# Kernel tuning notes

Measured on AMD Instinct MI355X. Metric: run time of the kernel, lower is better.

## Reference

```python
import math
import jax, jax.numpy as jnp
import numpy as np

NUM_BUCKETS = 32
MAX_DISTANCE = 128
N_HEADS = 16
D_KV = 64


def relative_position_bucket(rel_pos, num_buckets=NUM_BUCKETS, max_distance=MAX_DISTANCE):
    # bidirectional=True path of the original
    n = -rel_pos
    nb = num_buckets // 2
    ret = (n < 0).astype(jnp.int32) * nb
    n = jnp.abs(n)
    max_exact = nb // 2
    is_small = n < max_exact
    val_large = max_exact + (
        jnp.log(n.astype(jnp.float32) / max_exact)
        / math.log(max_distance / max_exact)
        * (nb - max_exact)
    ).astype(jnp.int32)
    val_large = jnp.minimum(val_large, nb - 1)
    return jnp.where(is_small, n, val_large) + ret


def setup_inputs() -> dict:
    key = jax.random.key(0)
    ks = jax.random.split(key, 6)
    B, S, D = 2, 2048, 1024
    inner = N_HEADS * D_KV  # 1024
    sc = 1.0 / math.sqrt(D)
    return {
        "x": jax.random.normal(ks[0], (B, S, D), dtype=jnp.float32),
        "Wq": jax.random.normal(ks[1], (D, inner), dtype=jnp.float32) * sc,
        "Wk": jax.random.normal(ks[2], (D, inner), dtype=jnp.float32) * sc,
        "Wv": jax.random.normal(ks[3], (D, inner), dtype=jnp.float32) * sc,
        "Wo": jax.random.normal(ks[4], (inner, D), dtype=jnp.float32) * sc,
        "rel_table": jax.random.normal(ks[5], (NUM_BUCKETS, N_HEADS), dtype=jnp.float32),
        "attention_mask": jnp.zeros((B, 1, 1, S), dtype=jnp.float32),
    }


def reference(x, Wq, Wk, Wv, Wo, rel_table, attention_mask):
    B, S, D = x.shape
    H, Dk = N_HEADS, D_KV

    q = (x @ Wq).reshape(B, S, H, Dk).transpose(0, 2, 1, 3)  # bhqd
    k = (x @ Wk).reshape(B, S, H, Dk).transpose(0, 2, 1, 3)
    v = (x @ Wv).reshape(B, S, H, Dk).transpose(0, 2, 1, 3)

    # NOTE: T5 attention has no 1/sqrt(d) scaling
    scores = jnp.einsum('bhqd,bhkd->bhqk', q.astype(jnp.float32), k.astype(jnp.float32))

    pos = jnp.arange(S)
    rel_pos = pos[None, :] - pos[:, None]  # [S,S] = k_pos - q_pos
    buckets = relative_position_bucket(rel_pos)
    position_bias = jnp.transpose(rel_table[buckets], (2, 0, 1))  # [H,S,S]

    scores = scores + position_bias[None, ...] + attention_mask
    weights = jax.nn.softmax(scores, axis=-1)
    out = jnp.einsum('bhqk,bhkd->bhqd', weights, v.astype(jnp.float32))
    out = out.transpose(0, 2, 1, 3).reshape(B, S, H * Dk).astype(x.dtype)
    out = out @ Wo
    return (out, position_bias)
```

## Files before the change

kernel.cpp:

```cpp
#include <hip/hip_runtime.h>
#include <hip/hip_bf16.h>
#include <math.h>
#include <stdint.h>

typedef __bf16 bf16_t;
typedef __attribute__((ext_vector_type(8))) __bf16 bf16x8;
typedef __attribute__((ext_vector_type(4))) float f32x4;
typedef float f32x4a __attribute__((ext_vector_type(4), aligned(4)));
typedef unsigned short u16;
typedef unsigned int u32;

#define DEV static __device__ __forceinline__
#define LOG2E 1.4426950408889634f

DEV u16 f2b(float f){ bf16_t h = (bf16_t)f; return __builtin_bit_cast(u16, h); }
DEV float b2f(u16 u){ bf16_t h = __builtin_bit_cast(bf16_t, u); return (float)h; }
DEV f32x4 mfma16(bf16x8 a, bf16x8 b, f32x4 c){
  return __builtin_amdgcn_mfma_f32_16x16x32_bf16(a, b, c, 0, 0, 0);
}

#if __has_builtin(__builtin_amdgcn_exp2f)
DEV float fexp2(float x){ return __builtin_amdgcn_exp2f(x); }
#else
DEV float fexp2(float x){ return exp2f(x); }
#endif

DEV void gld16(const void* g, void* l){
  __builtin_amdgcn_global_load_lds((const __attribute__((address_space(1))) u32*)g,
                                   (__attribute__((address_space(3))) u32*)l, 16, 0, 0);
}

DEV bf16x8 ldsA64(const u16* arr, int row, int ch){
  return *(const bf16x8*)&arr[row*64 + ((ch ^ (row&7))*8)];
}
DEV bf16x8 ldsA32(const u16* arr, int row, int ch){
  return *(const bf16x8*)&arr[row*32 + ((ch ^ ((row>>1)&3))*8)];
}

__global__ __launch_bounds__(256) void k_prep(const float* __restrict__ x,
                                              const float* __restrict__ Wq, const float* __restrict__ Wk,
                                              const float* __restrict__ Wv, const float* __restrict__ Wo,
                                              const float* __restrict__ rel_table, const float* __restrict__ mask,
                                              u16* __restrict__ xh, u16* __restrict__ xl,
                                              u16* __restrict__ wth, u16* __restrict__ wot,
                                              float* __restrict__ bt, float* __restrict__ bt2,
                                              float* __restrict__ msk2){
  __shared__ float tile[64][65];
  int bid = blockIdx.x;
  int t = threadIdx.x;
  if(bid < 4096){
    size_t i = ((size_t)bid*256 + t)*4;
    float4 v = *(const float4*)(x + i);
    ushort4 hv, lv; float f, hf;
    f=v.x; hv.x=f2b(f); hf=b2f(hv.x); lv.x=f2b(f-hf);
    f=v.y; hv.y=f2b(f); hf=b2f(hv.y); lv.y=f2b(f-hf);
    f=v.z; hv.z=f2b(f); hf=b2f(hv.z); lv.z=f2b(f-hf);
    f=v.w; hv.w=f2b(f); hf=b2f(hv.w); lv.w=f2b(f-hf);
    *(ushort4*)(xh+i) = hv;
    *(ushort4*)(xl+i) = lv;
  } else if(bid < 5120){
    int rr = bid - 4096;
    int z = rr >> 8, ky = (rr >> 4) & 15, nx = rr & 15;
    const float* W = (z==0)?Wq:((z==1)?Wk:((z==2)?Wv:Wo));
    int n0 = nx*64, k0 = ky*64;
    int r = t>>6, c = t&63;
    #pragma unroll
    for(int i=0;i<16;i++){
      int row = i*4 + r;
      tile[row][c] = W[(size_t)(k0+row)*1024 + n0 + c];
    }
    __syncthreads();
    #pragma unroll
    for(int i=0;i<16;i++){
      int nrow = i*4 + r;
      float v = tile[c][nrow];
      size_t o = (size_t)(n0+nrow)*1024 + k0 + c;
      if(z<3) wth[(size_t)z*1048576 + o] = f2b(v);
      else    wot[o] = f2b(v);
    }
  } else {
    int gid = (bid-5120)*256 + t;
    if(gid < 4096) msk2[gid] = mask[gid]*LOG2E;
    int h = gid >> 12, idx = gid & 4095;
    float v = 0.f;
    if(idx < 4095){
      int delta = idx - 2047;
      int n = -delta;
      int ret = 0;
      if(n < 0){ ret = 16; n = -n; }
      int bucket;
      if(n < 8) bucket = n + ret;
      else {
        float a = (float)log((double)n * 0.125);
        float rr2 = (float)((double)a / (double)2.7725887298583984f);
        int vl = 8 + (int)(rr2 * 8.0f);
        vl = vl > 15 ? 15 : vl;
        bucket = vl + ret;
      }
      v = rel_table[bucket*16 + h];
    }
    bt[gid] = v;
    bt2[gid] = v*LOG2E - 32.0f;
  }
}

__global__ __launch_bounds__(256) void k_gemm_qkv(const u16* __restrict__ xh, const u16* __restrict__ xl,
                                                  const u16* __restrict__ wth,
                                                  u16* __restrict__ qh, u16* __restrict__ ql,
                                                  u16* __restrict__ kh, u16* __restrict__ vt){
  __shared__ __align__(16) u16 SM[24576];
  int z = blockIdx.z;
  const u16* WH = wth + (size_t)z*1048576;
  int lin2 = blockIdx.x + 8*blockIdx.y;
  int nl2 = (lin2 & 7)*32 + (lin2 >> 3);
  int n0 = (nl2 & 7)*128, m0 = (nl2 >> 3)*128;
  int t = threadIdx.x, w = t>>6, lane = t&63, l16 = lane&15, g = lane>>4;
  f32x4 acc[4][4];
  #pragma unroll
  for(int i=0;i<4;i++)
    #pragma unroll
    for(int j=0;j<4;j++) acc[i][j] = {0.f,0.f,0.f,0.f};
  int rbase = (w>>1)*64, cbase = (w&1)*64;

  #pragma unroll
  for(int jj=0;jj<6;jj++){
    int q = w + 4*jj;
    int arr = q>>3, sub = q&7;
    if(z!=0 && arr==1) continue;
    int row = sub*16 + (lane>>2);
    int lch = (lane&3) ^ ((row>>1)&3);
    const u16* src;
    if(arr==0)      src = xh + (size_t)(m0+row)*1024 + lch*8;
    else if(arr==1) src = xl + (size_t)(m0+row)*1024 + lch*8;
    else            src = WH + (size_t)(n0+row)*1024 + lch*8;
    gld16(src, &SM[q*512]);
  }
  __syncthreads();

  for(int it=0; it<32; ++it){
    const u16* Ah = SM + (it&1)*12288;
    const u16* Al = Ah + 4096;
    const u16* Bh = Ah + 8192;
    if(it < 31){
      u16* dstb = SM + ((it+1)&1)*12288;
      int kn = (it+1)*32;
      #pragma unroll
      for(int jj=0;jj<6;jj++){
        int q = w + 4*jj;
        int arr = q>>3, sub = q&7;
        if(z!=0 && arr==1) continue;
        int row = sub*16 + (lane>>2);
        int lch = (lane&3) ^ ((row>>1)&3);
        const u16* src;
        if(arr==0)      src = xh + (size_t)(m0+row)*1024 + kn + lch*8;
        else if(arr==1) src = xl + (size_t)(m0+row)*1024 + kn + lch*8;
        else            src = WH + (size_t)(n0+row)*1024 + kn + lch*8;
        gld16(src, dstb + q*512);
      }
      __builtin_amdgcn_sched_barrier(0);
    }
    if(z!=0){
      bf16x8 ah[4];
      #pragma unroll
      for(int i=0;i<4;i++) ah[i] = ldsA32(Ah, rbase + i*16 + l16, g);
      #pragma unroll
      for(int j=0;j<4;j++){
        bf16x8 bh = ldsA32(Bh, cbase + j*16 + l16, g);
        #pragma unroll
        for(int i=0;i<4;i++)
          acc[i][j] = mfma16(ah[i], bh, acc[i][j]);
      }
    } else {
      bf16x8 ah[4], am[4];
      #pragma unroll
      for(int i=0;i<4;i++){
        int row = rbase + i*16 + l16;
        ah[i] = ldsA32(Ah, row, g);
        am[i] = ldsA32(Al, row, g);
      }
      #pragma unroll
      for(int j=0;j<4;j++){
        bf16x8 bh = ldsA32(Bh, cbase + j*16 + l16, g);
        #pragma unroll
        for(int i=0;i<4;i++){
          acc[i][j] = mfma16(ah[i], bh, acc[i][j]);
          acc[i][j] = mfma16(am[i], bh, acc[i][j]);
        }
      }
    }
    __syncthreads();
  }
  if(z==2){
    #pragma unroll
    for(int i=0;i<4;i++)
      #pragma unroll
      for(int j=0;j<4;j++)
        #pragma unroll
        for(int r=0;r<4;r++){
          int ml = rbase + i*16 + g*4 + r;
          int nl = cbase + j*16 + l16;
          SM[nl*136 + ml] = f2b(acc[i][j][r]);
        }
    __syncthreads();
    int bb = m0 >> 11;
    #pragma unroll
    for(int kk=0;kk<8;kk++){
      int id = t + 256*kk;
      int row = id>>4, ch = id&15;
      uint4 v = *(const uint4*)&SM[row*136 + ch*8];
      int n = n0 + row;
      size_t dst = ((size_t)(bb*16 + (n>>6))*64 + (n&63))*2048 + (m0&2047) + ch*8;
      *(uint4*)&vt[dst] = v;
    }
  } else {
    #pragma unroll
    for(int i=0;i<4;i++)
      #pragma unroll
      for(int j=0;j<4;j++)
        #pragma unroll
        for(int r=0;r<4;r++){
          int m = m0 + rbase + i*16 + g*4 + r;
          int n = n0 + cbase + j*16 + l16;
          float v = acc[i][j][r];
          if(z==0) v *= LOG2E;
          int b = m >> 11, s = m & 2047;
          int hh = n >> 6, d = n & 63;
          size_t a = ((size_t)(b*16+hh)*2048 + s)*64 + d;
          u16 hb = f2b(v);
          if(z==0){ qh[a]=hb; ql[a]=f2b(v - b2f(hb)); }
          else    { kh[a]=hb; }
        }
  }
}

__global__ __launch_bounds__(256,4) void k_attn(const u16* __restrict__ qh, const u16* __restrict__ ql,
                                              const u16* __restrict__ kh,
                                              const u16* __restrict__ vt, const float* __restrict__ bt2,
                                              const float* __restrict__ msk2,
                                              const float* __restrict__ bt, float* __restrict__ bias_out,
                                              u16* __restrict__ ao){
  __shared__ __align__(16) u16 SM[20480];
  int lin = blockIdx.x + 32*blockIdx.y;
  int nlw = (lin & 7)*128 + (lin >> 3);
  int qx = nlw & 31, bh = nlw >> 5;
  int b = bh>>4, h = bh&15;
  int q0 = qx*64;
  int t = threadIdx.x, w = t>>6, lane = t&63, l16 = lane&15, g = lane>>4;
  size_t base  = (size_t)bh*2048*64;
  size_t vbase = (size_t)bh*64*2048;
  u16* PSw = SM + 16384 + w*1024;
  const float* bt2h = bt2 + h*4096;
  const float* msk2b = msk2 + b*2048;
  size_t wbase = ((size_t)(bh*32 + qx))*65536 + t*8;

  bf16x8 qfh[2], qfl[2];
  {
    int qr = q0 + w*16 + l16;
    size_t a0 = base + (size_t)qr*64 + g*8;
    qfh[0] = *(const bf16x8*)&qh[a0];
    qfl[0] = *(const bf16x8*)&ql[a0];
    qfh[1] = *(const bf16x8*)&qh[a0+32];
    qfl[1] = *(const bf16x8*)&ql[a0+32];
  }
  f32x4 O[4];
  float rs[4];
  #pragma unroll
  for(int jd=0;jd<4;jd++) O[jd] = {0.f,0.f,0.f,0.f};
  #pragma unroll
  for(int r=0;r<4;r++) rs[r] = 0.f;
  int qgbase = q0 + w*16 + g*4;

  f32x4a bv0, bv1;
  {
    size_t f = wbase;
    int hh = (int)(f >> 22);
    int rem = (int)(f & 4194303);
    int qq = rem >> 11;
    int kk = rem & 2047;
    const float* row = bt + hh*4096 + (kk - qq + 2047);
    bv0 = *(const f32x4a*)(row);
    bv1 = *(const f32x4a*)(row + 4);
  }
  #pragma unroll
  for(int jj=0;jj<4;jj++){
    int q = w + 4*jj;
    int arr = q>>3, sub = q&7;
    int row = sub*8 + (lane>>3);
    int lch = (lane&7) ^ (row&7);
    const u16* src = (arr==0) ? kh + base + (size_t)row*64 + lch*8
                              : vt + vbase + (size_t)row*2048 + lch*8;
    gld16(src, &SM[q*512]);
  }
  __syncthreads();

  for(int it=0; it<32; ++it){
    int k0 = it*64;
    const u16* KH = SM + (it&1)*8192;
    const u16* VT = KH + 4096;
    if(it < 31){
      u16* dstb = SM + ((it+1)&1)*8192;
      int kn = k0 + 64;
      #pragma unroll
      for(int jj=0;jj<4;jj++){
        int q = w + 4*jj;
        int arr = q>>3, sub = q&7;
        int row = sub*8 + (lane>>3);
        int lch = (lane&7) ^ (row&7);
        const u16* src = (arr==0) ? kh + base + (size_t)(kn+row)*64 + lch*8
                                  : vt + vbase + (size_t)row*2048 + kn + lch*8;
        gld16(src, dstb + q*512);
      }
      __builtin_amdgcn_sched_barrier(0);
    }
    f32x4 sc[4];
    {
      const float* bb = bt2h + (k0 + l16 + 2047 - qgbase);
      #pragma unroll
      for(int j=0;j<4;j++){
        f32x4a ld = *(const f32x4a*)(bb + j*16 - 3);
        float mk = msk2b[k0 + j*16 + l16];
        sc[j] = (f32x4){ld[3]+mk, ld[2]+mk, ld[1]+mk, ld[0]+mk};
      }
    }
    {
      size_t f = wbase + (size_t)it*2048;
      __builtin_nontemporal_store(bv0, (f32x4a*)(bias_out + f));
      __builtin_nontemporal_store(bv1, (f32x4a*)(bias_out + f + 4));
      if(it < 31){
        size_t fn = f + 2048;
        int hh = (int)(fn >> 22);
        int rem = (int)(fn & 4194303);
        int qq = rem >> 11;
        int kk = rem & 2047;
        const float* row = bt + hh*4096 + (kk - qq + 2047);
        bv0 = *(const f32x4a*)(row);
        bv1 = *(const f32x4a*)(row + 4);
      }
    }
    __builtin_amdgcn_s_setprio(1);
    #pragma unroll
    for(int j=0;j<4;j++){
      int krow = j*16 + l16;
      bf16x8 kfh0 = ldsA64(KH, krow, g);
      bf16x8 kfh1 = ldsA64(KH, krow, 4+g);
      f32x4 s = sc[j];
      s = mfma16(qfh[0], kfh0, s);
      s = mfma16(qfl[0], kfh0, s);
      s = mfma16(qfh[1], kfh1, s);
      s = mfma16(qfl[1], kfh1, s);
      sc[j] = s;
    }
    __builtin_amdgcn_s_setprio(0);
    #pragma unroll
    for(int j=0;j<4;j++){
      #pragma unroll
      for(int r=0;r<4;r++){
        float p = fexp2(sc[j][r]);
        rs[r] += p;
        int rowp = g*4 + r;
        int colp = j*16 + l16;
        PSw[rowp*64 + (((colp>>3) ^ (rowp&7))*8) + (colp&7)] = f2b(p);
      }
    }
    __builtin_amdgcn_s_setprio(1);
    #pragma unroll
    for(int ds=0; ds<2; ds++){
      bf16x8 pa = ldsA64(PSw, l16, ds*4 + g);
      #pragma unroll
      for(int jd=0;jd<4;jd++){
        bf16x8 vb = ldsA64(VT, jd*16 + l16, ds*4 + g);
        O[jd] = mfma16(pa, vb, O[jd]);
      }
    }
    __builtin_amdgcn_s_setprio(0);
    __syncthreads();
  }
  #pragma unroll
  for(int r=0;r<4;r++){
    float v = rs[r];
    v += __shfl_xor(v,1,64);
    v += __shfl_xor(v,2,64);
    v += __shfl_xor(v,4,64);
    v += __shfl_xor(v,8,64);
    float inv = 1.f/v;
    int q = qgbase + r;
    size_t a = ((size_t)(b*2048 + q))*1024 + h*64;
    #pragma unroll
    for(int jd=0;jd<4;jd++)
      ao[a + jd*16 + l16] = f2b(O[jd][r]*inv);
  }
}

__global__ __launch_bounds__(256) void k_gemm_out(const u16* __restrict__ ao, const u16* __restrict__ wot,
                                                  float* __restrict__ out){
  __shared__ __align__(16) u16 SM[16384];
  int lin2 = blockIdx.x + 8*blockIdx.y;
  int nl2 = (lin2 & 7)*32 + (lin2 >> 3);
  int n0 = (nl2 & 7)*128, m0 = (nl2 >> 3)*128;
  int t = threadIdx.x, w = t>>6, lane = t&63, l16 = lane&15, g = lane>>4;
  f32x4 acc[4][4];
  #pragma unroll
  for(int i=0;i<4;i++)
    #pragma unroll
    for(int j=0;j<4;j++) acc[i][j] = {0.f,0.f,0.f,0.f};
  int rbase = (w>>1)*64, cbase = (w&1)*64;

  #pragma unroll
  for(int jj=0;jj<4;jj++){
    int q = w + 4*jj;
    int arr = q>>3, sub = q&7;
    int row = sub*16 + (lane>>2);
    int lch = (lane&3) ^ ((row>>1)&3);
    const u16* src = (arr==0) ? ao  + (size_t)(m0+row)*1024 + lch*8
                              : wot + (size_t)(n0+row)*1024 + lch*8;
    gld16(src, &SM[q*512]);
  }
  __syncthreads();

  for(int it=0; it<32; ++it){
    const u16* As = SM + (it&1)*8192;
    const u16* Bs = As + 4096;
    if(it < 31){
      u16* dstb = SM + ((it+1)&1)*8192;
      int kn = (it+1)*32;
      #pragma unroll
      for(int jj=0;jj<4;jj++){
        int q = w + 4*jj;
        int arr = q>>3, sub = q&7;
        int row = sub*16 + (lane>>2);
        int lch = (lane&3) ^ ((row>>1)&3);
        const u16* src = (arr==0) ? ao  + (size_t)(m0+row)*1024 + kn + lch*8
                                  : wot + (size_t)(n0+row)*1024 + kn + lch*8;
        gld16(src, dstb + q*512);
      }
      __builtin_amdgcn_sched_barrier(0);
    }
    bf16x8 af[4];
    #pragma unroll
    for(int i=0;i<4;i++) af[i] = ldsA32(As, rbase + i*16 + l16, g);
    #pragma unroll
    for(int j=0;j<4;j++){
      bf16x8 bfb = ldsA32(Bs, cbase + j*16 + l16, g);
      #pragma unroll
      for(int i=0;i<4;i++)
        acc[i][j] = mfma16(af[i], bfb, acc[i][j]);
    }
    __syncthreads();
  }
  #pragma unroll
  for(int i=0;i<4;i++)
    #pragma unroll
    for(int j=0;j<4;j++)
      #pragma unroll
      for(int r=0;r<4;r++){
        int m = m0 + rbase + i*16 + g*4 + r;
        int n = n0 + cbase + j*16 + l16;
        __builtin_nontemporal_store(acc[i][j][r], &out[(size_t)m*1024 + n]);
      }
}

extern "C" void kernel_launch(void* const* d_in, const int* in_sizes, int n_in,
                              void* d_out, int out_size, void* d_ws, size_t ws_size,
                              hipStream_t stream) {
  const float* x   = (const float*)d_in[0];
  const float* Wq  = (const float*)d_in[1];
  const float* Wk  = (const float*)d_in[2];
  const float* Wv  = (const float*)d_in[3];
  const float* Wo  = (const float*)d_in[4];
  const float* rel = (const float*)d_in[5];
  const float* msk = (const float*)d_in[6];
  float* out = (float*)d_out;
  float* bias_out = out + (size_t)4194304;
  char* ws = (char*)d_ws;
  u16* xh  = (u16*)(ws + 0);
  u16* xl  = (u16*)(ws + 8388608);
  u16* wth = (u16*)(ws + 16777216);
  u16* wot = (u16*)(ws + 23068672);
  u16* qh  = (u16*)(ws + 25165824);
  u16* ql  = (u16*)(ws + 33554432);
  u16* kh  = (u16*)(ws + 41943040);
  u16* vt  = (u16*)(ws + 50331648);
  u16* ao  = (u16*)(ws + 58720256);
  float* bt  = (float*)(ws + 67108864);
  float* bt2 = (float*)(ws + 67371008);
  float* msk2= (float*)(ws + 67633152);

  k_prep      <<<5376, 256, 0, stream>>>(x, Wq, Wk, Wv, Wo, rel, msk,
                                         xh, xl, wth, wot, bt, bt2, msk2);
  k_gemm_qkv  <<<dim3(8,32,3), 256, 0, stream>>>(xh, xl, wth, qh, ql, kh, vt);
  k_attn      <<<dim3(32,32), 256, 0, stream>>>(qh, ql, kh, vt, bt2, msk2, bt, bias_out, ao);
  k_gemm_out  <<<dim3(8,32), 256, 0, stream>>>(ao, wot, out);
}
```

Baseline: 442.3 us.

## Transpose QK MFMA operands in attention and shrink output GEMM N-tile

After: 435.9 us, median of 2. No clear change (-1.5%).

```diff
diff --git a/kernel.cpp b/kernel.cpp
--- a/kernel.cpp
+++ b/kernel.cpp
@@ -263,11 +263,11 @@
     qfl[1] = *(const bf16x8*)&ql[a0+32];
   }
   f32x4 O[4];
-  float rs[4];
+  float rs4[4];
   #pragma unroll
   for(int jd=0;jd<4;jd++) O[jd] = {0.f,0.f,0.f,0.f};
   #pragma unroll
-  for(int r=0;r<4;r++) rs[r] = 0.f;
+  for(int r=0;r<4;r++) rs4[r] = 0.f;
   int qgbase = q0 + w*16 + g*4;
 
   f32x4a bv0, bv1;
@@ -314,12 +314,13 @@
     }
     f32x4 sc[4];
     {
-      const float* bb = bt2h + (k0 + l16 + 2047 - qgbase);
+      const float* bb = bt2h + (k0 + g*4 + 2047 - (q0 + w*16 + l16));
+      const float* mm = msk2b + k0 + g*4;
       #pragma unroll
       for(int j=0;j<4;j++){
-        f32x4a ld = *(const f32x4a*)(bb + j*16 - 3);
-        float mk = msk2b[k0 + j*16 + l16];
-        sc[j] = (f32x4){ld[3]+mk, ld[2]+mk, ld[1]+mk, ld[0]+mk};
+        f32x4a bvv = *(const f32x4a*)(bb + j*16);
+        f32x4a mvv = *(const f32x4a*)(mm + j*16);
+        sc[j] = (f32x4){bvv[0]+mvv[0], bvv[1]+mvv[1], bvv[2]+mvv[2], bvv[3]+mvv[3]};
       }
     }
     {
@@ -344,23 +345,22 @@
       bf16x8 kfh0 = ldsA64(KH, krow, g);
       bf16x8 kfh1 = ldsA64(KH, krow, 4+g);
       f32x4 s = sc[j];
-      s = mfma16(qfh[0], kfh0, s);
-      s = mfma16(qfl[0], kfh0, s);
-      s = mfma16(qfh[1], kfh1, s);
-      s = mfma16(qfl[1], kfh1, s);
+      s = mfma16(kfh0, qfh[0], s);
+      s = mfma16(kfh0, qfl[0], s);
+      s = mfma16(kfh1, qfh[1], s);
+      s = mfma16(kfh1, qfl[1], s);
       sc[j] = s;
     }
     __builtin_amdgcn_s_setprio(0);
     #pragma unroll
     for(int j=0;j<4;j++){
-      #pragma unroll
-      for(int r=0;r<4;r++){
-        float p = fexp2(sc[j][r]);
-        rs[r] += p;
-        int rowp = g*4 + r;
-        int colp = j*16 + l16;
-        PSw[rowp*64 + (((colp>>3) ^ (rowp&7))*8) + (colp&7)] = f2b(p);
-      }
+      float p0 = fexp2(sc[j][0]); rs4[0] += p0;
+      float p1 = fexp2(sc[j][1]); rs4[1] += p1;
+      float p2 = fexp2(sc[j][2]); rs4[2] += p2;
+      float p3 = fexp2(sc[j][3]); rs4[3] += p3;
+      ushort4 us = { f2b(p0), f2b(p1), f2b(p2), f2b(p3) };
+      int ch = (j*2 + (g>>1)) ^ (l16 & 7);
+      *(ushort4*)&PSw[l16*64 + ch*8 + (g&1)*4] = us;
     }
     __builtin_amdgcn_s_setprio(1);
     #pragma unroll
@@ -375,14 +375,12 @@
     __builtin_amdgcn_s_setprio(0);
     __syncthreads();
   }
+  float tot = (rs4[0]+rs4[1]) + (rs4[2]+rs4[3]);
+  tot += __shfl_xor(tot, 16, 64);
+  tot += __shfl_xor(tot, 32, 64);
   #pragma unroll
   for(int r=0;r<4;r++){
-    float v = rs[r];
-    v += __shfl_xor(v,1,64);
-    v += __shfl_xor(v,2,64);
-    v += __shfl_xor(v,4,64);
-    v += __shfl_xor(v,8,64);
-    float inv = 1.f/v;
+    float inv = 1.f/__shfl(tot, g*4+r, 64);
     int q = qgbase + r;
     size_t a = ((size_t)(b*2048 + q))*1024 + h*64;
     #pragma unroll
@@ -393,20 +391,20 @@
 
 __global__ __launch_bounds__(256) void k_gemm_out(const u16* __restrict__ ao, const u16* __restrict__ wot,
                                                   float* __restrict__ out){
-  __shared__ __align__(16) u16 SM[16384];
-  int lin2 = blockIdx.x + 8*blockIdx.y;
-  int nl2 = (lin2 & 7)*32 + (lin2 >> 3);
-  int n0 = (nl2 & 7)*128, m0 = (nl2 >> 3)*128;
+  __shared__ __align__(16) u16 SM[12288];
+  int lin2 = blockIdx.x + 16*blockIdx.y;
+  int nl2 = (lin2 & 7)*64 + (lin2 >> 3);
+  int n0 = (nl2 & 15)*64, m0 = (nl2 >> 4)*128;
   int t = threadIdx.x, w = t>>6, lane = t&63, l16 = lane&15, g = lane>>4;
-  f32x4 acc[4][4];
+  f32x4 acc[4][2];
   #pragma unroll
   for(int i=0;i<4;i++)
     #pragma unroll
-    for(int j=0;j<4;j++) acc[i][j] = {0.f,0.f,0.f,0.f};
-  int rbase = (w>>1)*64, cbase = (w&1)*64;
-
-  #pragma unroll
-  for(int jj=0;jj<4;jj++){
+    for(int j=0;j<2;j++) acc[i][j] = {0.f,0.f,0.f,0.f};
+  int rbase = (w>>1)*64, cbase = (w&1)*32;
+
+  #pragma unroll
+  for(int jj=0;jj<3;jj++){
     int q = w + 4*jj;
     int arr = q>>3, sub = q&7;
     int row = sub*16 + (lane>>2);
@@ -418,13 +416,13 @@
   __syncthreads();
 
   for(int it=0; it<32; ++it){
-    const u16* As = SM + (it&1)*8192;
+    const u16* As = SM + (it&1)*6144;
     const u16* Bs = As + 4096;
     if(it < 31){
-      u16* dstb = SM + ((it+1)&1)*8192;
+      u16* dstb = SM + ((it+1)&1)*6144;
       int kn = (it+1)*32;
       #pragma unroll
-      for(int jj=0;jj<4;jj++){
+      for(int jj=0;jj<3;jj++){
         int q = w + 4*jj;
         int arr = q>>3, sub = q&7;
         int row = sub*16 + (lane>>2);
@@ -439,7 +437,7 @@
     #pragma unroll
     for(int i=0;i<4;i++) af[i] = ldsA32(As, rbase + i*16 + l16, g);
     #pragma unroll
-    for(int j=0;j<4;j++){
+    for(int j=0;j<2;j++){
       bf16x8 bfb = ldsA32(Bs, cbase + j*16 + l16, g);
       #pragma unroll
       for(int i=0;i<4;i++)
@@ -450,7 +448,7 @@
   #pragma unroll
   for(int i=0;i<4;i++)
     #pragma unroll
-    for(int j=0;j<4;j++)
+    for(int j=0;j<2;j++)
       #pragma unroll
       for(int r=0;r<4;r++){
         int m = m0 + rbase + i*16 + g*4 + r;
@@ -489,5 +487,5 @@
                                          xh, xl, wth, wot, bt, bt2, msk2);
   k_gemm_qkv  <<<dim3(8,32,3), 256, 0, stream>>>(xh, xl, wth, qh, ql, kh, vt);
   k_attn      <<<dim3(32,32), 256, 0, stream>>>(qh, ql, kh, vt, bt2, msk2, bt, bias_out, ao);
-  k_gemm_out  <<<dim3(8,32), 256, 0, stream>>>(ao, wot, out);
-}
+  k_gemm_out  <<<dim3(16,32), 256, 0, stream>>>(ao, wot, out);
+}
```
